# Kernel optimization log

Measured on AMD Instinct MI355X. Metric: run time of the kernel, lower is better.

The kernel has to match this reference:

```python
import jax, jax.numpy as jnp
import numpy as np

D_MODEL = 1024
NUM_HEADS = 16
D_K = D_MODEL // NUM_HEADS
B, T = 4, 2048


def setup_inputs() -> dict:
    key = jax.random.key(0)
    ks = jax.random.split(key, 10)
    s = 1.0 / np.sqrt(D_MODEL)
    return {
        "x": jax.random.normal(ks[0], (B, T, D_MODEL), dtype=jnp.float32),
        "attn_mask": jax.random.randint(ks[1], (B, T), 0, 2, dtype=jnp.int32),
        "wq": jax.random.uniform(ks[2], (D_MODEL, D_MODEL), jnp.float32, -s, s),
        "bq": jax.random.uniform(ks[3], (D_MODEL,), jnp.float32, -s, s),
        "wk": jax.random.uniform(ks[4], (D_MODEL, D_MODEL), jnp.float32, -s, s),
        "bk": jax.random.uniform(ks[5], (D_MODEL,), jnp.float32, -s, s),
        "wv": jax.random.uniform(ks[6], (D_MODEL, D_MODEL), jnp.float32, -s, s),
        "bv": jax.random.uniform(ks[7], (D_MODEL,), jnp.float32, -s, s),
        "wo": jax.random.uniform(ks[8], (D_MODEL, D_MODEL), jnp.float32, -s, s),
        "bo": jax.random.uniform(ks[9], (D_MODEL,), jnp.float32, -s, s),
    }


def reference(x, attn_mask, wq, bq, wk, bk, wv, bv, wo, bo):
    b, t, d = x.shape
    h, dk = NUM_HEADS, D_K
    # project and split heads: [B, H, T, Dk]
    q = (x @ wq + bq).reshape(b, t, h, dk).transpose(0, 2, 1, 3)
    k = (x @ wk + bk).reshape(b, t, h, dk).transpose(0, 2, 1, 3)
    v = (x @ wv + bv).reshape(b, t, h, dk).transpose(0, 2, 1, 3)
    scores = jnp.einsum("bhqd,bhkd->bhqk", q, k) / jnp.sqrt(jnp.float32(dk))
    mask = attn_mask[:, None, None, :]  # [B,1,1,T]
    scores = jnp.where(mask == 0, jnp.float32(-1e9), scores)
    attn = jax.nn.softmax(scores, axis=-1)
    out = jnp.einsum("bhqk,bhkd->bhqd", attn, v)
    out = out.transpose(0, 2, 1, 3).reshape(b, t, d)
    return out @ wo + bo
```

## Files before the change

### kernel.cpp

```cpp
#include <hip/hip_runtime.h>
#include <math.h>

#define TT 2048
#define DD 1024
#define HH 16
#define DKK 64
#define BB 4
#define NN 8192

typedef __bf16 bf16x8 __attribute__((ext_vector_type(8)));
typedef float f32x4 __attribute__((ext_vector_type(4)));
typedef float f32x16 __attribute__((ext_vector_type(16)));
typedef unsigned int uint2v __attribute__((ext_vector_type(2)));

#define QSCALE 0.18033688011112043f

__device__ __forceinline__ unsigned short f2bf(float f) {
  unsigned int u = __builtin_bit_cast(unsigned int, f);
  u += 0x7fffu + ((u >> 16) & 1u);
  return (unsigned short)(u >> 16);
}

__device__ __forceinline__ unsigned int cvtpk(float lo, float hi) {
  unsigned int r;
  asm("v_cvt_pk_bf16_f32 %0, %1, %2" : "=v"(r) : "v"(lo), "v"(hi));
  return r;
}

__device__ __forceinline__ void gl_lds16(const void* g, void* s) {
  __builtin_amdgcn_global_load_lds(
      (const __attribute__((address_space(1))) void*)g,
      (__attribute__((address_space(3))) void*)s, 16, 0, 0);
}

#define SWZ(r, byte) ((byte) ^ (((r) & 7) << 4))

__global__ __launch_bounds__(256) void cast_f32_bf16(
    const float* __restrict__ in, unsigned short* __restrict__ out, int n4) {
  int i = blockIdx.x * blockDim.x + threadIdx.x;
  if (i < n4) {
    float4 v = reinterpret_cast<const float4*>(in)[i];
    ushort4 o;
    o.x = f2bf(v.x); o.y = f2bf(v.y); o.z = f2bf(v.z); o.w = f2bf(v.w);
    reinterpret_cast<ushort4*>(out)[i] = o;
  }
}

__global__ __launch_bounds__(256) void wtrans(
    const float* __restrict__ W0, const float* __restrict__ W1,
    const float* __restrict__ W2, const float* __restrict__ W3,
    unsigned short* __restrict__ WT) {
  __shared__ float t[32][33];
  const float* W = (blockIdx.z == 0) ? W0
                   : (blockIdx.z == 1) ? W1
                   : (blockIdx.z == 2) ? W2 : W3;
  unsigned short* O = WT + (size_t)blockIdx.z * DD * DD;
  const int tx = threadIdx.x & 31, ty = threadIdx.x >> 5;
  const int r0 = blockIdx.y * 32, c0 = blockIdx.x * 32;
#pragma unroll
  for (int j = 0; j < 4; ++j)
    t[ty + 8 * j][tx] = W[(size_t)(r0 + ty + 8 * j) * DD + c0 + tx];
  __syncthreads();
#pragma unroll
  for (int j = 0; j < 4; ++j)
    O[(size_t)(c0 + ty + 8 * j) * DD + r0 + tx] = f2bf(t[tx][ty + 8 * j]);
}

__global__ __launch_bounds__(256) void mask_scan(
    const int* __restrict__ mask, int* __restrict__ rix, int* __restrict__ cnt) {
  __shared__ int part[256];
  const int b = blockIdx.x;
  const int tid = threadIdx.x;
  const int* mp = mask + b * TT;
  for (int i = tid; i < TT; i += 256) rix[b * TT + i] = 0;
  int loc[8], s = 0;
#pragma unroll
  for (int j = 0; j < 8; ++j) {
    loc[j] = mp[tid * 8 + j] ? 1 : 0;
    s += loc[j];
  }
  part[tid] = s;
  __syncthreads();
  for (int off = 1; off < 256; off <<= 1) {
    const int u = (tid >= off) ? part[tid - off] : 0;
    __syncthreads();
    part[tid] += u;
    __syncthreads();
  }
  if (tid == 255) cnt[b] = part[255];
  int run = part[tid] - s;
#pragma unroll
  for (int j = 0; j < 8; ++j) {
    if (loc[j]) rix[b * TT + run] = tid * 8 + j;
    run += loc[j];
  }
}

__global__ __launch_bounds__(512) void gemm_qkv256(
    const unsigned short* __restrict__ A, const unsigned short* __restrict__ Bw,
    const float* __restrict__ b0, const float* __restrict__ b1,
    const float* __restrict__ b2, const int* __restrict__ rix,
    const int* __restrict__ cnt, unsigned short* __restrict__ O0,
    unsigned short* __restrict__ O1, unsigned short* __restrict__ O2) {
  __shared__ unsigned short As[2][256 * 64];
  __shared__ unsigned short Bs[2][256 * 64];
  const int tid = threadIdx.x;
  const int l = tid & 63, w = tid >> 6;
  const int ln = l & 15, kg = l >> 4;
  const int wr = w >> 2, wc = w & 3;
  const int rb = blockIdx.x * 256;
  const int cb = blockIdx.y * 256;
  const int sel = blockIdx.y >> 2;
  const int b_ = rb >> 11;
  const int rbl = rb & 2047;

  const int sr = tid >> 3;
  const int sch = ((tid & 7) * 16) ^ ((sr & 7) << 4);

  const char* Ag[4];
  if (sel > 0) {
    if (rbl >= cnt[b_]) return;
    const int* rixb = rix + (b_ << 11);
#pragma unroll
    for (int j = 0; j < 4; ++j) {
      const int r = rixb[rbl + j * 64 + sr];
      Ag[j] = (const char*)A + ((size_t)((b_ << 11) + r) * 2048) + sch;
    }
  } else {
#pragma unroll
    for (int j = 0; j < 4; ++j)
      Ag[j] = (const char*)A + ((size_t)(rb + j * 64 + sr) * 2048) + sch;
  }
  const char* Bg[4];
#pragma unroll
  for (int j = 0; j < 4; ++j)
    Bg[j] = (const char*)Bw + ((size_t)(cb + j * 64 + sr) * 2048) + sch;

  f32x4 acc[8][4];
#pragma unroll
  for (int i = 0; i < 8; ++i)
#pragma unroll
    for (int j = 0; j < 4; ++j)
#pragma unroll
      for (int r = 0; r < 4; ++r) acc[i][j][r] = 0.f;

#pragma unroll
  for (int j = 0; j < 4; ++j) {
    gl_lds16(Ag[j], (char*)As[0] + j * 8192 + w * 1024);
    gl_lds16(Bg[j], (char*)Bs[0] + j * 8192 + w * 1024);
  }
  __syncthreads();

  int cur = 0;
  for (int t = 0; t < 16; ++t) {
    if (t < 15) {
      const int kb = (t + 1) * 128;
#pragma unroll
      for (int j = 0; j < 4; ++j) {
        gl_lds16(Ag[j] + kb, (char*)As[cur ^ 1] + j * 8192 + w * 1024);
        gl_lds16(Bg[j] + kb, (char*)Bs[cur ^ 1] + j * 8192 + w * 1024);
      }
    }
#pragma unroll
    for (int ks = 0; ks < 2; ++ks) {
      bf16x8 bfv[4];
#pragma unroll
      for (int ni = 0; ni < 4; ++ni) {
        const int row = wc * 64 + ni * 16 + ln;
        bfv[ni] = *reinterpret_cast<const bf16x8*>(
            (const char*)Bs[cur] + row * 128 + SWZ(row, ks * 64 + kg * 16));
      }
#pragma unroll
      for (int mi = 0; mi < 8; ++mi) {
        const int row = wr * 128 + mi * 16 + ln;
        const bf16x8 af = *reinterpret_cast<const bf16x8*>(
            (const char*)As[cur] + row * 128 + SWZ(row, ks * 64 + kg * 16));
#pragma unroll
        for (int ni = 0; ni < 4; ++ni)
          acc[mi][ni] = __builtin_amdgcn_mfma_f32_16x16x32_bf16(
              af, bfv[ni], acc[mi][ni], 0, 0, 0);
      }
    }
    __syncthreads();
    cur ^= 1;
  }

  const float* bias = sel == 0 ? b0 : (sel == 1 ? b1 : b2);
  const float scale = sel == 0 ? QSCALE : 1.0f;
  const int bhb = b_ * HH;
#pragma unroll
  for (int ni = 0; ni < 4; ++ni) {
    const int c3 = cb + wc * 64 + ni * 16 + ln;
    const int c = c3 & 1023, h = (c3 >> 6) & 15, dk = c3 & 63;
    const float bsv = bias[c];
    const int bh = bhb + h;
#pragma unroll
    for (int mi = 0; mi < 8; ++mi) {
#pragma unroll
      for (int r = 0; r < 4; ++r) {
        const int rl = rbl + wr * 128 + mi * 16 + kg * 4 + r;
        const unsigned short v = f2bf((acc[mi][ni][r] + bsv) * scale);
        if (sel == 0) {
          O0[(size_t)(bh * 16 + (rl >> 7)) * 8192 + (dk >> 3) * 1024 +
             (rl & 127) * 8 + (dk & 7)] = v;
        } else if (sel == 1) {
          O1[(size_t)(bh * 32 + (rl >> 6)) * 4096 + (dk >> 3) * 512 +
             ((rl >> 5) & 1) * 256 + (rl & 31) * 8 + (dk & 7)] = v;
        } else {
          O2[(size_t)(bh * 32 + (rl >> 6)) * 4096 + ((rl >> 3) & 7) * 512 +
             (dk >> 5) * 256 + (dk & 31) * 8 + (rl & 7)] = v;
        }
      }
    }
  }
}

__global__ __launch_bounds__(256) void gemm_out(
    const unsigned short* __restrict__ A, const unsigned short* __restrict__ Bw,
    const float* __restrict__ bias, float* __restrict__ Of) {
  __shared__ unsigned short As[2][128 * 64];
  __shared__ unsigned short Bs[2][128 * 64];
  const int tid = threadIdx.x;
  const int l = tid & 63, w = tid >> 6;
  const int ln = l & 15, kg = l >> 4;
  const int wr = w >> 1, wc = w & 1;
  const int rb = blockIdx.x * 128, cb = blockIdx.y * 128;

  const int sr = w * 8 + (l >> 3);
  const int sch = ((l & 7) * 16) ^ (((l >> 3) & 7) << 4);

  const char* Ag[4];
  const char* Bg[4];
#pragma unroll
  for (int j = 0; j < 4; ++j) {
    Ag[j] = (const char*)A + ((size_t)(rb + j * 32 + sr) * 2048) + sch;
    Bg[j] = (const char*)Bw + ((size_t)(cb + j * 32 + sr) * 2048) + sch;
  }

  f32x4 acc[4][4];
#pragma unroll
  for (int i = 0; i < 4; ++i)
#pragma unroll
    for (int j = 0; j < 4; ++j)
#pragma unroll
      for (int r = 0; r < 4; ++r) acc[i][j][r] = 0.f;

#pragma unroll
  for (int j = 0; j < 4; ++j) {
    gl_lds16(Ag[j], (char*)As[0] + j * 4096 + w * 1024);
    gl_lds16(Bg[j], (char*)Bs[0] + j * 4096 + w * 1024);
  }
  __syncthreads();

  int cur = 0;
  for (int t = 0; t < 16; ++t) {
    if (t < 15) {
      const int kb = (t + 1) * 128;
#pragma unroll
      for (int j = 0; j < 4; ++j) {
        gl_lds16(Ag[j] + kb, (char*)As[cur ^ 1] + j * 4096 + w * 1024);
        gl_lds16(Bg[j] + kb, (char*)Bs[cur ^ 1] + j * 4096 + w * 1024);
      }
    }
#pragma unroll
    for (int ks = 0; ks < 2; ++ks) {
      bf16x8 af[4], bfv[4];
#pragma unroll
      for (int mi = 0; mi < 4; ++mi) {
        const int row = wr * 64 + mi * 16 + ln;
        af[mi] = *reinterpret_cast<const bf16x8*>(
            (const char*)As[cur] + row * 128 + SWZ(row, ks * 64 + kg * 16));
      }
#pragma unroll
      for (int ni = 0; ni < 4; ++ni) {
        const int row = wc * 64 + ni * 16 + ln;
        bfv[ni] = *reinterpret_cast<const bf16x8*>(
            (const char*)Bs[cur] + row * 128 + SWZ(row, ks * 64 + kg * 16));
      }
#pragma unroll
      for (int mi = 0; mi < 4; ++mi)
#pragma unroll
        for (int ni = 0; ni < 4; ++ni)
          acc[mi][ni] = __builtin_amdgcn_mfma_f32_16x16x32_bf16(
              af[mi], bfv[ni], acc[mi][ni], 0, 0, 0);
    }
    __syncthreads();
    cur ^= 1;
  }

#pragma unroll
  for (int ni = 0; ni < 4; ++ni) {
    const int cl = cb + wc * 64 + ni * 16 + ln;
    const float bsv = bias[cl];
#pragma unroll
    for (int mi = 0; mi < 4; ++mi)
#pragma unroll
      for (int r = 0; r < 4; ++r) {
        const int rl = rb + wr * 64 + mi * 16 + kg * 4 + r;
        Of[(size_t)rl * DD + cl] = acc[mi][ni][r] + bsv;
      }
  }
}

template <bool TAIL>
__device__ __forceinline__ void attn_tile10(
    int kt, int n, const char* __restrict__ KU, const char* __restrict__ VU,
    int foff, int hi, const bf16x8 (&qf)[4], f32x16& oc0, f32x16& oc1,
    float& l_) {
  const int ktoff = kt << 13;

  f32x16 sc0, sc1;
#pragma unroll
  for (int i = 0; i < 16; ++i) { sc0[i] = 0.f; sc1[i] = 0.f; }
  __builtin_amdgcn_s_setprio(1);
#pragma unroll
  for (int s = 0; s < 4; ++s) {
    const bf16x8 kf0 =
        *reinterpret_cast<const bf16x8*>(KU + ktoff + foff + s * 2048);
    const bf16x8 kf1 =
        *reinterpret_cast<const bf16x8*>(KU + ktoff + foff + s * 2048 + 512);
    sc0 = __builtin_amdgcn_mfma_f32_32x32x16_bf16(kf0, qf[s], sc0, 0, 0, 0);
    sc1 = __builtin_amdgcn_mfma_f32_32x32x16_bf16(kf1, qf[s], sc1, 0, 0, 0);
  }
  __builtin_amdgcn_s_setprio(0);

  bf16x8 vf[8];
#pragma unroll
  for (int s = 0; s < 4; ++s) {
    vf[2 * s] = *reinterpret_cast<const bf16x8*>(VU + ktoff + foff + s * 2048);
    vf[2 * s + 1] =
        *reinterpret_cast<const bf16x8*>(VU + ktoff + foff + s * 2048 + 512);
  }

#pragma unroll
  for (int i = 0; i < 16; ++i) sc0[i] = __builtin_exp2f(sc0[i]);
#pragma unroll
  for (int i = 0; i < 16; ++i) sc1[i] = __builtin_exp2f(sc1[i]);

  if (TAIL) {
    const int kvb = (kt << 6) + 4 * hi;
#pragma unroll
    for (int i = 0; i < 16; ++i) {
      const int kv0 = kvb + (i & 3) + 8 * (i >> 2);
      sc0[i] = (kv0 < n) ? sc0[i] : 0.f;
      sc1[i] = (kv0 + 32 < n) ? sc1[i] : 0.f;
    }
  }

  {
    const float ra = ((sc0[0] + sc0[1]) + (sc0[2] + sc0[3])) +
                     ((sc0[4] + sc0[5]) + (sc0[6] + sc0[7]));
    const float rb2 = ((sc0[8] + sc0[9]) + (sc0[10] + sc0[11])) +
                      ((sc0[12] + sc0[13]) + (sc0[14] + sc0[15]));
    const float rc = ((sc1[0] + sc1[1]) + (sc1[2] + sc1[3])) +
                     ((sc1[4] + sc1[5]) + (sc1[6] + sc1[7]));
    const float rd = ((sc1[8] + sc1[9]) + (sc1[10] + sc1[11])) +
                     ((sc1[12] + sc1[13]) + (sc1[14] + sc1[15]));
    l_ += (ra + rb2) + (rc + rd);
  }

  bf16x8 pf[4];
#pragma unroll
  for (int s = 0; s < 4; ++s) {
    const int u = s & 1;
    float p0, p1, p2, p3, p4, p5, p6, p7;
    if ((s >> 1) == 0) {
      p0 = sc0[8 * u + 0]; p1 = sc0[8 * u + 1]; p2 = sc0[8 * u + 2];
      p3 = sc0[8 * u + 3]; p4 = sc0[8 * u + 4]; p5 = sc0[8 * u + 5];
      p6 = sc0[8 * u + 6]; p7 = sc0[8 * u + 7];
    } else {
      p0 = sc1[8 * u + 0]; p1 = sc1[8 * u + 1]; p2 = sc1[8 * u + 2];
      p3 = sc1[8 * u + 3]; p4 = sc1[8 * u + 4]; p5 = sc1[8 * u + 5];
      p6 = sc1[8 * u + 6]; p7 = sc1[8 * u + 7];
    }
    const unsigned int wa0 = cvtpk(p0, p1), wa1 = cvtpk(p2, p3);
    const unsigned int wb0 = cvtpk(p4, p5), wb1 = cvtpk(p6, p7);
    const uint2v r0 = __builtin_amdgcn_permlane32_swap(wa0, wb0, false, false);
    const uint2v r1 = __builtin_amdgcn_permlane32_swap(wa1, wb1, false, false);
    union { unsigned int u4[4]; bf16x8 v; } pw;
    pw.u4[0] = r0.x;
    pw.u4[1] = r1.x;
    pw.u4[2] = r0.y;
    pw.u4[3] = r1.y;
    pf[s] = pw.v;
  }

  __builtin_amdgcn_s_setprio(1);
#pragma unroll
  for (int s = 0; s < 4; ++s) {
    oc0 = __builtin_amdgcn_mfma_f32_32x32x16_bf16(vf[2 * s], pf[s], oc0, 0, 0, 0);
    oc1 = __builtin_amdgcn_mfma_f32_32x32x16_bf16(vf[2 * s + 1], pf[s], oc1, 0, 0, 0);
  }
  __builtin_amdgcn_s_setprio(0);
}

__global__ __launch_bounds__(256) void attn_v10(
    const unsigned short* __restrict__ Qt, const unsigned short* __restrict__ Kt,
    const unsigned short* __restrict__ Vt, const int* __restrict__ cnt,
    unsigned short* __restrict__ Ab) {
  const int id = blockIdx.x + 16 * blockIdx.y;
  const int bh = id & 63, qt = id >> 6;
  const int b = bh >> 4, h = bh & 15;

  __shared__ __align__(16) char lds[16384];

  const int tid = threadIdx.x;
  const int l = tid & 63, w = tid >> 6;
  const int ln = l & 31, hi = l >> 5;

  const char* Qtile = (const char*)Qt + (size_t)(bh * 16 + qt) * 16384;
  const char* KU = (const char*)Kt + ((size_t)bh << 18);
  const char* VU = (const char*)Vt + ((size_t)bh << 18);
  const int n = cnt[b];
  const int ntile = (n > 0) ? ((n + 63) >> 6) : 1;

  const int qrow = w * 32 + ln;
  bf16x8 qf[4];
#pragma unroll
  for (int s = 0; s < 4; ++s)
    qf[s] = *reinterpret_cast<const bf16x8*>(
        Qtile + (size_t)(s * 2 + hi) * 2048 + qrow * 16);

  const int foff = hi * 1024 + ln * 16;

  f32x16 oc0, oc1;
#pragma unroll
  for (int i = 0; i < 16; ++i) { oc0[i] = 0.f; oc1[i] = 0.f; }
  float l_ = 0.f;

  for (int kt = 0; kt + 1 < ntile; ++kt)
    attn_tile10<false>(kt, n, KU, VU, foff, hi, qf, oc0, oc1, l_);
  attn_tile10<true>(ntile - 1, n, KU, VU, foff, hi, qf, oc0, oc1, l_);

  float ls = l_ + __shfl_xor(l_, 32);
  const float inv = 1.0f / ls;
#pragma unroll
  for (int i = 0; i < 16; ++i) { oc0[i] *= inv; oc1[i] *= inv; }
#pragma unroll
  for (int g = 0; g < 4; ++g) {
    const int d0a = 8 * g + 4 * hi;
    uint2 wv;
    wv.x = cvtpk(oc0[4 * g + 0], oc0[4 * g + 1]);
    wv.y = cvtpk(oc0[4 * g + 2], oc0[4 * g + 3]);
    *reinterpret_cast<uint2*>(lds + qrow * 128 + SWZ(qrow, d0a * 2)) = wv;
    uint2 wv1;
    wv1.x = cvtpk(oc1[4 * g + 0], oc1[4 * g + 1]);
    wv1.y = cvtpk(oc1[4 * g + 2], oc1[4 * g + 3]);
    *reinterpret_cast<uint2*>(lds + qrow * 128 + SWZ(qrow, 64 + d0a * 2)) = wv1;
  }
  __syncthreads();
  {
    const int row2 = tid >> 1, halfc = tid & 1;
    char* gout = (char*)Ab + ((size_t)(b * TT + qt * 128 + row2)) * 2048 +
                 h * 128 + halfc * 64;
#pragma unroll
    for (int u2 = 0; u2 < 4; ++u2) {
      const uint4 d4 = *reinterpret_cast<const uint4*>(
          lds + row2 * 128 + SWZ(row2, halfc * 64 + u2 * 16));
      *reinterpret_cast<uint4*>(gout + u2 * 16) = d4;
    }
  }
}

extern "C" void kernel_launch(void* const* d_in, const int* in_sizes, int n_in,
                              void* d_out, int out_size, void* d_ws,
                              size_t ws_size, hipStream_t stream) {
  const float* x = (const float*)d_in[0];
  const int* attn_mask = (const int*)d_in[1];
  const float* wq = (const float*)d_in[2];
  const float* bq = (const float*)d_in[3];
  const float* wk = (const float*)d_in[4];
  const float* bk = (const float*)d_in[5];
  const float* wv = (const float*)d_in[6];
  const float* bv = (const float*)d_in[7];
  const float* wo = (const float*)d_in[8];
  const float* bo = (const float*)d_in[9];
  float* out = (float*)d_out;

  unsigned short* Xb = (unsigned short*)d_ws;
  unsigned short* WT = Xb + (size_t)NN * DD;
  unsigned short* Qt = WT + (size_t)4 * DD * DD;
  unsigned short* Kt = Qt + (size_t)NN * DD;
  unsigned short* Vt = Kt + (size_t)NN * DD;
  unsigned short* Ab = Vt + (size_t)NN * DD;
  int* rix = (int*)(Ab + (size_t)NN * DD);
  int* cnt = rix + (size_t)BB * TT;

  cast_f32_bf16<<<(NN * DD / 4 + 255) / 256, 256, 0, stream>>>(
      x, Xb, NN * DD / 4);
  wtrans<<<dim3(DD / 32, DD / 32, 4), 256, 0, stream>>>(wq, wk, wv, wo, WT);
  mask_scan<<<BB, 256, 0, stream>>>(attn_mask, rix, cnt);

  gemm_qkv256<<<dim3(NN / 256, 12), 512, 0, stream>>>(
      Xb, WT, bq, bk, bv, rix, cnt, Qt, Kt, Vt);
  attn_v10<<<dim3(TT / 128, BB * HH), 256, 0, stream>>>(Qt, Kt, Vt, cnt, Ab);
  gemm_out<<<dim3(NN / 128, 8), 256, 0, stream>>>(
      Ab, WT + (size_t)3 * DD * DD, bo, out);
}
```

Measured before the change: 191.0 us.

## Restructure QKV GEMM mainloop into a deeper pipeline with split barriers

The QKV projection GEMM now loads two K-tiles ahead and waits on them with explicit vmcnt waits and raw s_barrier instead of __syncthreads. Each iteration pulls all A/B fragments for both k-substeps into registers up front, then issues the next tile's global-to-LDS loads between the two MFMA halves. It also adds s_setprio around the MFMA bursts. LDS is reorganised into one 128KB buffer laid out in half-tile blocks. The aim is to hide global load latency and barrier stalls better, at the cost of more registers and LDS and a more fragile hand-tuned ordering.

```diff
diff --git a/kernel.cpp b/kernel.cpp
--- a/kernel.cpp
+++ b/kernel.cpp
@@ -96,14 +96,13 @@
   }
 }
 
-__global__ __launch_bounds__(512) void gemm_qkv256(
+__global__ __launch_bounds__(512) void gemm_qkv8p(
     const unsigned short* __restrict__ A, const unsigned short* __restrict__ Bw,
     const float* __restrict__ b0, const float* __restrict__ b1,
     const float* __restrict__ b2, const int* __restrict__ rix,
     const int* __restrict__ cnt, unsigned short* __restrict__ O0,
     unsigned short* __restrict__ O1, unsigned short* __restrict__ O2) {
-  __shared__ unsigned short As[2][256 * 64];
-  __shared__ unsigned short Bs[2][256 * 64];
+  __shared__ __align__(16) char lds[131072];
   const int tid = threadIdx.x;
   const int l = tid & 63, w = tid >> 6;
   const int ln = l & 15, kg = l >> 4;
@@ -111,79 +110,118 @@
   const int rb = blockIdx.x * 256;
   const int cb = blockIdx.y * 256;
   const int sel = blockIdx.y >> 2;
-  const int b_ = rb >> 11;
-  const int rbl = rb & 2047;
-
-  const int sr = tid >> 3;
-  const int sch = ((tid & 7) * 16) ^ ((sr & 7) << 4);
+  const int b_ = rb >> 11, rbl = rb & 2047;
+
+  const int sr8 = tid >> 3;
+  const int sch = ((tid & 7) * 16) ^ ((sr8 & 7) << 4);
 
   const char* Ag[4];
   if (sel > 0) {
     if (rbl >= cnt[b_]) return;
     const int* rixb = rix + (b_ << 11);
 #pragma unroll
-    for (int j = 0; j < 4; ++j) {
-      const int r = rixb[rbl + j * 64 + sr];
-      Ag[j] = (const char*)A + ((size_t)((b_ << 11) + r) * 2048) + sch;
-    }
+    for (int h = 0; h < 2; ++h)
+#pragma unroll
+      for (int j = 0; j < 2; ++j) {
+        const int r = rixb[rbl + h * 128 + j * 64 + sr8];
+        Ag[h * 2 + j] =
+            (const char*)A + ((size_t)((b_ << 11) + r) * 2048) + sch;
+      }
   } else {
 #pragma unroll
+    for (int h = 0; h < 2; ++h)
+#pragma unroll
+      for (int j = 0; j < 2; ++j)
+        Ag[h * 2 + j] = (const char*)A +
+                        ((size_t)(rb + h * 128 + j * 64 + sr8) * 2048) + sch;
+  }
+  const char* Bg[4];
+#pragma unroll
+  for (int h = 0; h < 2; ++h)
+#pragma unroll
+    for (int j = 0; j < 2; ++j)
+      Bg[h * 2 + j] = (const char*)Bw +
+                      ((size_t)(cb + h * 128 + j * 64 + sr8) * 2048) + sch;
+
+#define STAGE(d_, kt_)                                                    \
+  {                                                                       \
+    const int kb_ = (kt_) * 128;                                          \
+    _Pragma("unroll") for (int h = 0; h < 2; ++h) {                       \
+      _Pragma("unroll") for (int j = 0; j < 2; ++j) {                     \
+        char* dst = lds + (d_) * 32768 + h * 16384 + (j * 64 + w * 8) * 128; \
+        gl_lds16(Ag[h * 2 + j] + kb_, dst);                               \
+        gl_lds16(Bg[h * 2 + j] + kb_, dst + 65536);                       \
+      }                                                                   \
+    }                                                                     \
+  }
+
+  f32x4 acc[8][4];
+#pragma unroll
+  for (int i = 0; i < 8; ++i)
+#pragma unroll
     for (int j = 0; j < 4; ++j)
-      Ag[j] = (const char*)A + ((size_t)(rb + j * 64 + sr) * 2048) + sch;
-  }
-  const char* Bg[4];
-#pragma unroll
-  for (int j = 0; j < 4; ++j)
-    Bg[j] = (const char*)Bw + ((size_t)(cb + j * 64 + sr) * 2048) + sch;
-
-  f32x4 acc[8][4];
-#pragma unroll
-  for (int i = 0; i < 8; ++i)
-#pragma unroll
-    for (int j = 0; j < 4; ++j)
 #pragma unroll
       for (int r = 0; r < 4; ++r) acc[i][j][r] = 0.f;
 
-#pragma unroll
-  for (int j = 0; j < 4; ++j) {
-    gl_lds16(Ag[j], (char*)As[0] + j * 8192 + w * 1024);
-    gl_lds16(Bg[j], (char*)Bs[0] + j * 8192 + w * 1024);
-  }
-  __syncthreads();
-
-  int cur = 0;
-  for (int t = 0; t < 16; ++t) {
-    if (t < 15) {
-      const int kb = (t + 1) * 128;
-#pragma unroll
-      for (int j = 0; j < 4; ++j) {
-        gl_lds16(Ag[j] + kb, (char*)As[cur ^ 1] + j * 8192 + w * 1024);
-        gl_lds16(Bg[j] + kb, (char*)Bs[cur ^ 1] + j * 8192 + w * 1024);
-      }
-    }
-#pragma unroll
-    for (int ks = 0; ks < 2; ++ks) {
-      bf16x8 bfv[4];
-#pragma unroll
-      for (int ni = 0; ni < 4; ++ni) {
-        const int row = wc * 64 + ni * 16 + ln;
-        bfv[ni] = *reinterpret_cast<const bf16x8*>(
-            (const char*)Bs[cur] + row * 128 + SWZ(row, ks * 64 + kg * 16));
-      }
-#pragma unroll
-      for (int mi = 0; mi < 8; ++mi) {
-        const int row = wr * 128 + mi * 16 + ln;
-        const bf16x8 af = *reinterpret_cast<const bf16x8*>(
-            (const char*)As[cur] + row * 128 + SWZ(row, ks * 64 + kg * 16));
-#pragma unroll
-        for (int ni = 0; ni < 4; ++ni)
-          acc[mi][ni] = __builtin_amdgcn_mfma_f32_16x16x32_bf16(
-              af, bfv[ni], acc[mi][ni], 0, 0, 0);
-      }
-    }
-    __syncthreads();
-    cur ^= 1;
-  }
+  STAGE(0, 0);
+  STAGE(1, 1);
+
+  const int brow = (wc & 1) * 64;
+  for (int kt = 0; kt < 16; ++kt) {
+    const int d = kt & 1;
+    if (kt < 15) {
+      asm volatile("s_waitcnt vmcnt(8)" ::: "memory");
+    } else {
+      asm volatile("s_waitcnt vmcnt(0)" ::: "memory");
+    }
+    __builtin_amdgcn_s_barrier();
+    __builtin_amdgcn_sched_barrier(0);
+
+    const char* Abase = lds + d * 32768 + wr * 16384;
+    const char* Bbase = lds + 65536 + d * 32768 + (wc >> 1) * 16384;
+    bf16x8 afr[8][2], bfr[4][2];
+#pragma unroll
+    for (int ni = 0; ni < 4; ++ni) {
+      const int row = brow + ni * 16 + ln;
+#pragma unroll
+      for (int ks = 0; ks < 2; ++ks)
+        bfr[ni][ks] = *reinterpret_cast<const bf16x8*>(
+            Bbase + row * 128 + SWZ(row, ks * 64 + kg * 16));
+    }
+#pragma unroll
+    for (int mi = 0; mi < 8; ++mi) {
+      const int row = mi * 16 + ln;
+#pragma unroll
+      for (int ks = 0; ks < 2; ++ks)
+        afr[mi][ks] = *reinterpret_cast<const bf16x8*>(
+            Abase + row * 128 + SWZ(row, ks * 64 + kg * 16));
+    }
+
+    __builtin_amdgcn_s_setprio(1);
+#pragma unroll
+    for (int mi = 0; mi < 8; ++mi)
+#pragma unroll
+      for (int ni = 0; ni < 4; ++ni)
+        acc[mi][ni] = __builtin_amdgcn_mfma_f32_16x16x32_bf16(
+            afr[mi][0], bfr[ni][0], acc[mi][ni], 0, 0, 0);
+    __builtin_amdgcn_s_setprio(0);
+
+    asm volatile("s_waitcnt lgkmcnt(0)" ::: "memory");
+    __builtin_amdgcn_sched_barrier(0);
+    __builtin_amdgcn_s_barrier();
+    if (kt + 2 < 16) STAGE(d, kt + 2);
+    __builtin_amdgcn_sched_barrier(0);
+
+    __builtin_amdgcn_s_setprio(1);
+#pragma unroll
+    for (int mi = 0; mi < 8; ++mi)
+#pragma unroll
+      for (int ni = 0; ni < 4; ++ni)
+        acc[mi][ni] = __builtin_amdgcn_mfma_f32_16x16x32_bf16(
+            afr[mi][1], bfr[ni][1], acc[mi][ni], 0, 0, 0);
+    __builtin_amdgcn_s_setprio(0);
+  }
+#undef STAGE
 
   const float* bias = sel == 0 ? b0 : (sel == 1 ? b1 : b2);
   const float scale = sel == 0 ? QSCALE : 1.0f;
@@ -491,7 +529,7 @@
   wtrans<<<dim3(DD / 32, DD / 32, 4), 256, 0, stream>>>(wq, wk, wv, wo, WT);
   mask_scan<<<BB, 256, 0, stream>>>(attn_mask, rix, cnt);
 
-  gemm_qkv256<<<dim3(NN / 256, 12), 512, 0, stream>>>(
+  gemm_qkv8p<<<dim3(NN / 256, 12), 512, 0, stream>>>(
       Xb, WT, bq, bk, bv, rix, cnt, Qt, Kt, Vt);
   attn_v10<<<dim3(TT / 128, BB * HH), 256, 0, stream>>>(Qt, Kt, Vt, cnt, Ab);
   gemm_out<<<dim3(NN / 128, 8), 256, 0, stream>>>(
```

Measured after the change: 183.3 us. 1.04x faster.
